# Optimization experiments

Measured on AMD Instinct MI355X. Metric: run time of the kernel, lower is better.

The kernel has to match this reference:

```python
import jax, jax.numpy as jnp
import numpy as np

N_HEADS = 16

def setup_inputs() -> dict:
    key = jax.random.key(0)
    ks = jax.random.split(key, 7)
    B, S, D = 2, 2048, 1024
    sc = 1.0 / np.sqrt(D)
    return {
        "x": jax.random.normal(ks[0], (B, S, D), dtype=jnp.float32),
        "Wq": jax.random.normal(ks[1], (D, D), dtype=jnp.float32) * sc,
        "bq": jax.random.normal(ks[2], (D,), dtype=jnp.float32) * 0.02,
        "Wk": jax.random.normal(ks[3], (D, D), dtype=jnp.float32) * sc,
        "bk": jax.random.normal(ks[4], (D,), dtype=jnp.float32) * 0.02,
        "Wv": jax.random.normal(ks[5], (D, D), dtype=jnp.float32) * sc,
        "bv": jax.random.normal(ks[6], (D,), dtype=jnp.float32) * 0.02,
    }

def reference(x, Wq, bq, Wk, bk, Wv, bv):
    B, S, D = x.shape
    H = N_HEADS
    W = D // H  # head width
    # QKV projections (torch Linear: x @ W^T + b); here weights stored as [D_in, D_out]
    q = x @ Wq + bq
    k = x @ Wk + bk
    v = x @ Wv + bv
    # split last dim into heads -> [B, H, S, W]
    q = q.reshape(B, S, H, W).transpose(0, 2, 1, 3)
    k = k.reshape(B, S, H, W).transpose(0, 2, 1, 3)
    v = v.reshape(B, S, H, W).transpose(0, 2, 1, 3)
    # scaled dot-product attention; full [B,H,S,S] scores as in original
    scores = jnp.einsum("bhqw,bhkw->bhqk", q, k) / jnp.sqrt(jnp.asarray(W, x.dtype))
    probs = jax.nn.softmax(scores, axis=-1)  # dropout is identity in eval mode
    h = jnp.einsum("bhqk,bhkw->bhqw", probs, v)
    # merge heads -> [B, S, D]
    return h.transpose(0, 2, 1, 3).reshape(B, S, D)
```

## Files before the change

kernel.cpp:

```cpp
#include <hip/hip_runtime.h>

typedef _Float16 H16;
typedef _Float16 half8 __attribute__((ext_vector_type(8)));
typedef _Float16 half4 __attribute__((ext_vector_type(4)));
typedef float f32x4 __attribute__((ext_vector_type(4)));

constexpr int Bb = 2, S = 2048, D = 1024, NH = 16, HW = 64;
constexpr int M = Bb * S;

constexpr size_t XH_OFF = 0;
constexpr size_t WT_OFF = XH_OFF + (size_t)M * D * 2;
constexpr size_t Q_OFF  = WT_OFF + 3ull * D * D * 2;
constexpr size_t K_OFF  = Q_OFF + (size_t)M * D * 2;
constexpr size_t VT_OFF = K_OFF + (size_t)M * D * 2;

#define GLOAD_LDS16(g, l)                                        \
  __builtin_amdgcn_global_load_lds(                              \
      (const __attribute__((address_space(1))) void*)(g),        \
      (__attribute__((address_space(3))) void*)(l), 16, 0, 0)

__global__ __launch_bounds__(256) void prep(const float* __restrict__ x,
                                            H16* __restrict__ xh,
                                            const float* __restrict__ w0,
                                            const float* __restrict__ w1,
                                            const float* __restrict__ w2,
                                            H16* __restrict__ wt) {
  __shared__ H16 tile[64][65];
  const int z = blockIdx.z;
  const int t = threadIdx.x;
  if (z == 0) {
    const int bid = blockIdx.y * 16 + blockIdx.x;
#pragma unroll
    for (int r = 0; r < 8; ++r) {
      size_t i = ((size_t)(bid * 8 + r) * 256 + t) * 8;
      float4 a = *(const float4*)(x + i);
      float4 b = *(const float4*)(x + i + 4);
      half8 h = {(H16)a.x, (H16)a.y, (H16)a.z, (H16)a.w,
                 (H16)b.x, (H16)b.y, (H16)b.z, (H16)b.w};
      *(half8*)(xh + i) = h;
    }
  } else {
    const float* w = z == 1 ? w0 : z == 2 ? w1 : w2;
    H16* out = wt + (size_t)(z - 1) * D * D;
    int c = t & 63, r4 = t >> 6;
    int bx = blockIdx.x * 64, by = blockIdx.y * 64;
#pragma unroll 4
    for (int it = 0; it < 16; ++it) {
      int row = it * 4 + r4;
      tile[c][row] = (H16)w[(size_t)(by + row) * D + bx + c];
    }
    __syncthreads();
#pragma unroll 4
    for (int it = 0; it < 16; ++it) {
      int row = it * 4 + r4;
      out[(size_t)(bx + row) * D + by + c] = tile[row][c];
    }
  }
}

__global__ __launch_bounds__(256) void qkv_gemm(
    const H16* __restrict__ xh, const H16* __restrict__ wt,
    const float* __restrict__ bq, const float* __restrict__ bk,
    const float* __restrict__ bv, H16* __restrict__ qo, H16* __restrict__ ko,
    H16* __restrict__ vto) {
  __shared__ __align__(16) H16 As[128 * 32];
  __shared__ __align__(16) H16 Bs[128 * 32];
  const int z = blockIdx.z;
  const H16* w = wt + (size_t)z * D * D;
  const float* bias = z == 0 ? bq : z == 1 ? bk : bv;
  const int bm = blockIdx.y * 128, bn = blockIdx.x * 128;
  const int t = threadIdx.x;
  const int wave = t >> 6, lane = t & 63;
  const int g = lane >> 4, c = lane & 15;
  const int wm = (wave >> 1) * 64, wn = (wave & 1) * 64;

  f32x4 acc[4][4] = {};

  for (int kk = 0; kk < D; kk += 32) {
#pragma unroll
    for (int rnd = 0; rnd < 2; ++rnd) {
      int cid = rnd * 256 + t;
      int row = cid >> 2, k0 = (cid & 3) * 8;
      GLOAD_LDS16(&xh[(size_t)(bm + row) * D + kk + k0], &As[cid * 8]);
      GLOAD_LDS16(&w[(size_t)(bn + row) * D + kk + k0], &Bs[cid * 8]);
    }
    __syncthreads();
    half8 af[4], bf[4];
#pragma unroll
    for (int i = 0; i < 4; ++i) {
      af[i] = *(const half8*)&As[(wm + i * 16 + c) * 32 + g * 8];
      bf[i] = *(const half8*)&Bs[(wn + i * 16 + c) * 32 + g * 8];
    }
#pragma unroll
    for (int i = 0; i < 4; ++i)
#pragma unroll
      for (int j = 0; j < 4; ++j)
        acc[i][j] =
            __builtin_amdgcn_mfma_f32_16x16x32_f16(af[i], bf[j], acc[i][j], 0, 0, 0);
    __syncthreads();
  }

#pragma unroll
  for (int i = 0; i < 4; ++i) {
#pragma unroll
    for (int j = 0; j < 4; ++j) {
      int coln = bn + wn + j * 16 + c;
      float bse = bias[coln];
      int h = coln >> 6, wcol = coln & 63;
      if (z == 2) {
        int row0 = bm + wm + i * 16 + g * 4;
        int bbx = row0 >> 11, s0 = row0 & (S - 1);
        half4 v4 = {(H16)(acc[i][j][0] + bse), (H16)(acc[i][j][1] + bse),
                    (H16)(acc[i][j][2] + bse), (H16)(acc[i][j][3] + bse)};
        *(half4*)&vto[((size_t)(bbx * NH + h) * HW + wcol) * S + s0] = v4;
      } else {
#pragma unroll
        for (int r = 0; r < 4; ++r) {
          int row = bm + wm + i * 16 + g * 4 + r;
          float val = acc[i][j][r] + bse;
          int bbx = row >> 11, s = row & (S - 1);
          size_t bh = (size_t)(bbx * NH + h);
          if (z == 0)
            qo[(bh * S + s) * HW + wcol] = (H16)val;
          else
            ko[(bh * S + s) * HW + wcol] = (H16)val;
        }
      }
    }
  }
}

__global__ __launch_bounds__(256, 2) void attn(const H16* __restrict__ q,
                                               const H16* __restrict__ k,
                                               const H16* __restrict__ vt,
                                               float* __restrict__ out) {
  constexpr int NIT = S / 64;
  __shared__ __align__(16) H16 Ks[2][64 * 64];
  __shared__ __align__(16) H16 Vs[2][64 * 64];
  __shared__ __align__(16) H16 pl[4][32 * 64];

  const int id = blockIdx.x;
  const int xcd = id & 7, slot = id >> 3;
  const int bh = xcd * 4 + (slot >> 4);
  const int qt = slot & 15;

  const int t = threadIdx.x, wave = t >> 6, lane = t & 63;
  const int g = lane >> 4, c = lane & 15;
  const int q0 = qt * 128 + wave * 32;
  const H16* qp = q + ((size_t)bh * S + q0) * HW;
  const H16* kp = k + (size_t)bh * S * HW;
  const H16* vp = vt + (size_t)bh * HW * S;

  const int r0 = t >> 3, k8 = t & 7;
  const int r1 = r0 + 32;
  const int wsw0 = r0 * 64 + ((k8 ^ (r0 & 7)) * 8);
  const int wsw1 = r1 * 64 + ((k8 ^ (r1 & 7)) * 8);

  const H16 scq = (H16)(0.125f * 1.44269504088896f);
  half8 qb[2][2];
#pragma unroll
  for (int qg = 0; qg < 2; ++qg) {
    qb[qg][0] = *(const half8*)&qp[(qg * 16 + c) * HW + g * 8];
    qb[qg][1] = *(const half8*)&qp[(qg * 16 + c) * HW + 32 + g * 8];
#pragma unroll
    for (int e = 0; e < 8; ++e) {
      qb[qg][0][e] *= scq;
      qb[qg][1][e] *= scq;
    }
  }

  f32x4 o[4][2] = {};
  float l[2] = {0.f, 0.f};
  H16* myp = pl[wave];

  const int sw0 = (g ^ (c & 7)) * 8;
  const int sw1 = ((4 + g) ^ (c & 7)) * 8;
  int pwc[4];
#pragma unroll
  for (int kt = 0; kt < 4; ++kt)
    pwc[kt] = (((kt * 2 + (g >> 1)) ^ (c & 7)) * 8) + (g & 1) * 4;

  {
    half8 ka = *(const half8*)&kp[(size_t)r0 * HW + k8 * 8];
    half8 kb = *(const half8*)&kp[(size_t)r1 * HW + k8 * 8];
    half8 va = *(const half8*)&vp[(size_t)r0 * S + k8 * 8];
    half8 vb = *(const half8*)&vp[(size_t)r1 * S + k8 * 8];
    *(half8*)&Ks[0][wsw0] = ka;
    *(half8*)&Ks[0][wsw1] = kb;
    *(half8*)&Vs[0][wsw0] = va;
    *(half8*)&Vs[0][wsw1] = vb;
  }

  int buf = 0;
  for (int it = 0; it < NIT; ++it) {
    __syncthreads();

    half8 nka, nkb, nva, nvb;
    if (it + 1 < NIT) {
      const int nck = (it + 1) * 64;
      nka = *(const half8*)&kp[(size_t)(nck + r0) * HW + k8 * 8];
      nkb = *(const half8*)&kp[(size_t)(nck + r1) * HW + k8 * 8];
      nva = *(const half8*)&vp[(size_t)r0 * S + nck + k8 * 8];
      nvb = *(const half8*)&vp[(size_t)r1 * S + nck + k8 * 8];
    }

    const H16* ks = Ks[buf];
    const H16* vs = Vs[buf];

    f32x4 st[4][2];
#pragma unroll
    for (int kt = 0; kt < 4; ++kt) {
      const H16* kr = &ks[(kt * 16 + c) * 64];
      half8 ka0 = *(const half8*)&kr[sw0];
      half8 ka1 = *(const half8*)&kr[sw1];
#pragma unroll
      for (int qg = 0; qg < 2; ++qg) {
        f32x4 z = {};
        st[kt][qg] =
            __builtin_amdgcn_mfma_f32_16x16x32_f16(ka0, qb[qg][0], z, 0, 0, 0);
        st[kt][qg] = __builtin_amdgcn_mfma_f32_16x16x32_f16(ka1, qb[qg][1],
                                                            st[kt][qg], 0, 0, 0);
      }
    }

    half8 pb[2][2];
#pragma unroll
    for (int qg = 0; qg < 2; ++qg) {
#pragma unroll
      for (int kt = 0; kt < 4; ++kt) {
        float p0 = __builtin_amdgcn_exp2f(st[kt][qg][0]);
        float p1 = __builtin_amdgcn_exp2f(st[kt][qg][1]);
        float p2 = __builtin_amdgcn_exp2f(st[kt][qg][2]);
        float p3 = __builtin_amdgcn_exp2f(st[kt][qg][3]);
        l[qg] += (p0 + p1) + (p2 + p3);
        half4 pk = {(H16)p0, (H16)p1, (H16)p2, (H16)p3};
        *(half4*)&myp[(qg * 16 + c) * 64 + pwc[kt]] = pk;
      }
      pb[qg][0] = *(const half8*)&myp[(qg * 16 + c) * 64 + sw0];
      pb[qg][1] = *(const half8*)&myp[(qg * 16 + c) * 64 + sw1];
    }

#pragma unroll
    for (int wt = 0; wt < 4; ++wt) {
      const H16* vr = &vs[(wt * 16 + c) * 64];
      half8 va0 = *(const half8*)&vr[sw0];
      half8 va1 = *(const half8*)&vr[sw1];
#pragma unroll
      for (int qg = 0; qg < 2; ++qg) {
        o[wt][qg] = __builtin_amdgcn_mfma_f32_16x16x32_f16(va0, pb[qg][0],
                                                           o[wt][qg], 0, 0, 0);
        o[wt][qg] = __builtin_amdgcn_mfma_f32_16x16x32_f16(va1, pb[qg][1],
                                                           o[wt][qg], 0, 0, 0);
      }
    }

    if (it + 1 < NIT) {
      H16* kd = Ks[buf ^ 1];
      H16* vd = Vs[buf ^ 1];
      *(half8*)&kd[wsw0] = nka;
      *(half8*)&kd[wsw1] = nkb;
      *(half8*)&vd[wsw0] = nva;
      *(half8*)&vd[wsw1] = nvb;
    }
    buf ^= 1;
  }

#pragma unroll
  for (int qg = 0; qg < 2; ++qg) {
    l[qg] += __shfl_xor(l[qg], 16, 64);
    l[qg] += __shfl_xor(l[qg], 32, 64);
  }

  const int bbx = bh >> 4, h = bh & 15;
#pragma unroll
  for (int qg = 0; qg < 2; ++qg) {
    const float inv = 1.0f / l[qg];
    float* orow = out + ((size_t)bbx * S + q0 + qg * 16 + c) * D + h * HW;
#pragma unroll
    for (int wt = 0; wt < 4; ++wt) {
      float4 v4 = {o[wt][qg][0] * inv, o[wt][qg][1] * inv, o[wt][qg][2] * inv,
                   o[wt][qg][3] * inv};
      *(float4*)&orow[wt * 16 + g * 4] = v4;
    }
  }
}

extern "C" void kernel_launch(void* const* d_in, const int* in_sizes, int n_in,
                              void* d_out, int out_size, void* d_ws,
                              size_t ws_size, hipStream_t stream) {
  const float* x = (const float*)d_in[0];
  const float* Wq = (const float*)d_in[1];
  const float* bq = (const float*)d_in[2];
  const float* Wk = (const float*)d_in[3];
  const float* bk = (const float*)d_in[4];
  const float* Wv = (const float*)d_in[5];
  const float* bv = (const float*)d_in[6];
  float* out = (float*)d_out;
  char* ws = (char*)d_ws;
  H16* xh = (H16*)(ws + XH_OFF);
  H16* wt = (H16*)(ws + WT_OFF);
  H16* qw = (H16*)(ws + Q_OFF);
  H16* kw = (H16*)(ws + K_OFF);
  H16* vtw = (H16*)(ws + VT_OFF);

  prep<<<dim3(16, 16, 4), 256, 0, stream>>>(x, xh, Wq, Wk, Wv, wt);
  qkv_gemm<<<dim3(8, 32, 3), 256, 0, stream>>>(xh, wt, bq, bk, bv, qw, kw, vtw);
  attn<<<dim3(512), 256, 0, stream>>>(qw, kw, vtw, out);
}
```

Baseline: 166.0 us.

## Split attention key range in two and merge partials in a combine kernel

The attention kernel now splits each query tile's key range into two halves, doubling the grid to 1024 blocks. Each block writes an unnormalized fp16 partial output and a row-sum to workspace, and a new combine kernel adds the two halves, normalizes and writes the fp32 output. Launch bounds are raised to 4 blocks per CU, and the per-wave P staging buffer is halved by reusing it across query groups. The aim is more parallelism and occupancy across the CUs, at the cost of an extra kernel launch and partial-result traffic to and from global memory.

After: 179.3 us. 8.0% more time.

```diff
diff --git a/kernel.cpp b/kernel.cpp
--- a/kernel.cpp
+++ b/kernel.cpp
@@ -13,6 +13,9 @@
 constexpr size_t Q_OFF  = WT_OFF + 3ull * D * D * 2;
 constexpr size_t K_OFF  = Q_OFF + (size_t)M * D * 2;
 constexpr size_t VT_OFF = K_OFF + (size_t)M * D * 2;
+constexpr size_t PO_OFF = VT_OFF + (size_t)M * D * 2;
+constexpr size_t PL_OFF = PO_OFF + 2ull * M * D * 2;
+constexpr int NQ = Bb * NH * S;
 
 #define GLOAD_LDS16(g, l)                                        \
   __builtin_amdgcn_global_load_lds(                              \
@@ -130,19 +133,22 @@
   }
 }
 
-__global__ __launch_bounds__(256, 2) void attn(const H16* __restrict__ q,
+__global__ __launch_bounds__(256, 4) void attn(const H16* __restrict__ q,
                                                const H16* __restrict__ k,
                                                const H16* __restrict__ vt,
-                                               float* __restrict__ out) {
-  constexpr int NIT = S / 64;
+                                               H16* __restrict__ pO,
+                                               float* __restrict__ pL) {
+  constexpr int NIT = 1024 / 64;
   __shared__ __align__(16) H16 Ks[2][64 * 64];
   __shared__ __align__(16) H16 Vs[2][64 * 64];
-  __shared__ __align__(16) H16 pl[4][32 * 64];
+  __shared__ __align__(16) H16 pl[4][16 * 64];
 
   const int id = blockIdx.x;
-  const int xcd = id & 7, slot = id >> 3;
-  const int bh = xcd * 4 + (slot >> 4);
-  const int qt = slot & 15;
+  const int xcd = id & 7, r = id >> 3;
+  const int sp = r & 1;
+  const int qt = (r >> 1) & 15;
+  const int bh = xcd * 4 + (r >> 5);
+  const int kb = sp * 1024;
 
   const int t = threadIdx.x, wave = t >> 6, lane = t & 63;
   const int g = lane >> 4, c = lane & 15;
@@ -181,12 +187,12 @@
     pwc[kt] = (((kt * 2 + (g >> 1)) ^ (c & 7)) * 8) + (g & 1) * 4;
 
   {
-    half8 ka = *(const half8*)&kp[(size_t)r0 * HW + k8 * 8];
-    half8 kb = *(const half8*)&kp[(size_t)r1 * HW + k8 * 8];
-    half8 va = *(const half8*)&vp[(size_t)r0 * S + k8 * 8];
-    half8 vb = *(const half8*)&vp[(size_t)r1 * S + k8 * 8];
+    half8 ka = *(const half8*)&kp[(size_t)(kb + r0) * HW + k8 * 8];
+    half8 kb8 = *(const half8*)&kp[(size_t)(kb + r1) * HW + k8 * 8];
+    half8 va = *(const half8*)&vp[(size_t)r0 * S + kb + k8 * 8];
+    half8 vb = *(const half8*)&vp[(size_t)r1 * S + kb + k8 * 8];
     *(half8*)&Ks[0][wsw0] = ka;
-    *(half8*)&Ks[0][wsw1] = kb;
+    *(half8*)&Ks[0][wsw1] = kb8;
     *(half8*)&Vs[0][wsw0] = va;
     *(half8*)&Vs[0][wsw1] = vb;
   }
@@ -197,7 +203,7 @@
 
     half8 nka, nkb, nva, nvb;
     if (it + 1 < NIT) {
-      const int nck = (it + 1) * 64;
+      const int nck = kb + (it + 1) * 64;
       nka = *(const half8*)&kp[(size_t)(nck + r0) * HW + k8 * 8];
       nkb = *(const half8*)&kp[(size_t)(nck + r1) * HW + k8 * 8];
       nva = *(const half8*)&vp[(size_t)r0 * S + nck + k8 * 8];
@@ -234,10 +240,10 @@
         float p3 = __builtin_amdgcn_exp2f(st[kt][qg][3]);
         l[qg] += (p0 + p1) + (p2 + p3);
         half4 pk = {(H16)p0, (H16)p1, (H16)p2, (H16)p3};
-        *(half4*)&myp[(qg * 16 + c) * 64 + pwc[kt]] = pk;
+        *(half4*)&myp[c * 64 + pwc[kt]] = pk;
       }
-      pb[qg][0] = *(const half8*)&myp[(qg * 16 + c) * 64 + sw0];
-      pb[qg][1] = *(const half8*)&myp[(qg * 16 + c) * 64 + sw1];
+      pb[qg][0] = *(const half8*)&myp[c * 64 + sw0];
+      pb[qg][1] = *(const half8*)&myp[c * 64 + sw1];
     }
 
 #pragma unroll
@@ -271,18 +277,39 @@
     l[qg] += __shfl_xor(l[qg], 32, 64);
   }
 
+  H16* po = pO + (size_t)sp * M * D;
+  float* plo = pL + (size_t)sp * NQ;
+#pragma unroll
+  for (int qg = 0; qg < 2; ++qg) {
+    const size_t qi = (size_t)bh * S + q0 + qg * 16 + c;
+#pragma unroll
+    for (int wt = 0; wt < 4; ++wt) {
+      half4 v4 = {(H16)o[wt][qg][0], (H16)o[wt][qg][1], (H16)o[wt][qg][2],
+                  (H16)o[wt][qg][3]};
+      *(half4*)&po[qi * HW + wt * 16 + g * 4] = v4;
+    }
+    if (g == 0) plo[qi] = l[qg];
+  }
+}
+
+__global__ __launch_bounds__(256) void combine(const H16* __restrict__ pO,
+                                               const float* __restrict__ pL,
+                                               float* __restrict__ out) {
+  const int gid = blockIdx.x * 256 + threadIdx.x;
+  const int qi = gid >> 3;
+  const int d8 = gid & 7;
+  half8 a = *(const half8*)&pO[(size_t)qi * HW + d8 * 8];
+  half8 b = *(const half8*)&pO[(size_t)M * D + (size_t)qi * HW + d8 * 8];
+  const float inv = 1.0f / (pL[qi] + pL[NQ + qi]);
+  const int bh = qi >> 11, s = qi & (S - 1);
   const int bbx = bh >> 4, h = bh & 15;
-#pragma unroll
-  for (int qg = 0; qg < 2; ++qg) {
-    const float inv = 1.0f / l[qg];
-    float* orow = out + ((size_t)bbx * S + q0 + qg * 16 + c) * D + h * HW;
-#pragma unroll
-    for (int wt = 0; wt < 4; ++wt) {
-      float4 v4 = {o[wt][qg][0] * inv, o[wt][qg][1] * inv, o[wt][qg][2] * inv,
-                   o[wt][qg][3] * inv};
-      *(float4*)&orow[wt * 16 + g * 4] = v4;
-    }
-  }
+  float* orow = out + ((size_t)bbx * S + s) * D + h * HW + d8 * 8;
+  float4 v0 = {((float)a[0] + (float)b[0]) * inv, ((float)a[1] + (float)b[1]) * inv,
+               ((float)a[2] + (float)b[2]) * inv, ((float)a[3] + (float)b[3]) * inv};
+  float4 v1 = {((float)a[4] + (float)b[4]) * inv, ((float)a[5] + (float)b[5]) * inv,
+               ((float)a[6] + (float)b[6]) * inv, ((float)a[7] + (float)b[7]) * inv};
+  *(float4*)&orow[0] = v0;
+  *(float4*)&orow[4] = v1;
 }
 
 extern "C" void kernel_launch(void* const* d_in, const int* in_sizes, int n_in,
@@ -302,8 +329,11 @@
   H16* qw = (H16*)(ws + Q_OFF);
   H16* kw = (H16*)(ws + K_OFF);
   H16* vtw = (H16*)(ws + VT_OFF);
+  H16* po = (H16*)(ws + PO_OFF);
+  float* plw = (float*)(ws + PL_OFF);
 
   prep<<<dim3(16, 16, 4), 256, 0, stream>>>(x, xh, Wq, Wk, Wv, wt);
   qkv_gemm<<<dim3(8, 32, 3), 256, 0, stream>>>(xh, wt, bq, bk, bv, qw, kw, vtw);
-  attn<<<dim3(512), 256, 0, stream>>>(qw, kw, vtw, out);
-}
+  attn<<<dim3(1024), 256, 0, stream>>>(qw, kw, vtw, po, plw);
+  combine<<<dim3(2048), 256, 0, stream>>>(po, plw, out);
+}
```
